# Kernel tuning notes

Measured on AMD Instinct MI355X. Metric: run time of the kernel, lower is better.

Reference implementation:

```python
import jax, jax.numpy as jnp
import numpy as np

N = 8192      # number of input points
K = 16        # nsample for all kNN groupings
STRIDE = 4    # TransitionDown stride -> M = N // 4 output points


def _knn(q, p, k):
    # squared euclidean distances [m, n] -> k nearest indices per query
    d2 = jnp.sum(q * q, 1)[:, None] + jnp.sum(p * p, 1)[None, :] - 2.0 * (q @ p.T)
    return jax.lax.top_k(-d2, k)[1]


def _forward(points, We1, se1, be1, We2, se2, be2,
             Wq1, Wk1, Wv1, sa1, ba1, Wq2, Wk2, Wv2, sa2, ba2,
             Wtd, sd, bd, Wu1, su1, bu1, Wu2, su2, bu2,
             Wc1, bc1, sc, bc, Wc2, bc2):
    p = points[0]                      # [N, 3]
    n = p.shape[0]
    idx = _knn(p, p, K)                # [N, K] shared xyz-kNN (same coords every layer)

    def edge_conv(x, W, s, b):
        # DGCNN EdgeConv: concat(x_i, x_j - x_i) -> Linear -> BN(affine) -> ReLU -> max_k
        xi = x[:, None, :]
        xj = x[idx]                    # [N, K, C]
        e = jnp.concatenate([jnp.broadcast_to(xi, xj.shape), xj - xi], -1)
        h = jax.nn.relu((e @ W) * s + b)
        return h.max(axis=1)

    def graph_attn(x, Wq, Wk, Wv, s, b):
        q, kk, v = x @ Wq, x @ Wk, x @ Wv
        kj, vj = kk[idx], v[idx]       # [N, K, D]
        logits = jnp.einsum('nd,nkd->nk', q, kj) / jnp.sqrt(jnp.float32(q.shape[-1]))
        a = jax.nn.softmax(logits, axis=-1)
        y = jnp.einsum('nk,nkd->nd', a, vj)
        return jax.nn.relu(y * s + b)

    x = edge_conv(p, We1, se1, be1)            # 3 -> 64
    x = edge_conv(x, We2, se2, be2)            # 64 -> 128
    x = graph_attn(x, Wq1, Wk1, Wv1, sa1, ba1) # 128 -> 256
    x = graph_attn(x, Wq2, Wk2, Wv2, sa2, ba2) # 256 -> 512

    # TransitionDown: subsample n/stride points, group kNN with relative xyz, MLP, max-pool
    sel = jnp.arange(0, n, STRIDE)
    pm = p[sel]                                 # [M, 3]
    idx_d = _knn(pm, p, K)                      # [M, K]
    g = jnp.concatenate([p[idx_d] - pm[:, None, :], x[idx_d]], -1)  # [M, K, 3+512]
    xd = jax.nn.relu((g @ Wtd) * sd + bd).max(axis=1)               # [M, 512]

    # TransitionUp(x, o): local linear + broadcast per-cloud pooled branch (single cloud, o=[n])
    gmean = xd.mean(axis=0, keepdims=True)
    xu = jax.nn.relu((xd @ Wu1) * su1 + bu1 + (gmean @ Wu2) * su2 + bu2)  # [M, 256]

    # classifier (eval mode: dropout = identity, BN folded to affine)
    h = jax.nn.relu(((xu @ Wc1) + bc1) * sc + bc)
    return h @ Wc2 + bc2               # [M, num_classes]


def setup_inputs() -> dict:
    key = jax.random.key(0)
    ks = iter(jax.random.split(key, 64))
    def w(shape):
        return jax.random.normal(next(ks), shape, jnp.float32) / jnp.sqrt(jnp.float32(shape[0]))
    def s(d):
        return 1.0 + 0.01 * jax.random.normal(next(ks), (d,), jnp.float32)
    def b(d):
        return 0.01 * jax.random.normal(next(ks), (d,), jnp.float32)
    return {
        'points': jax.random.normal(next(ks), (1, N, 3), jnp.float32),
        'We1': w((6, 64)), 'se1': s(64), 'be1': b(64),
        'We2': w((128, 128)), 'se2': s(128), 'be2': b(128),
        'Wq1': w((128, 256)), 'Wk1': w((128, 256)), 'Wv1': w((128, 256)), 'sa1': s(256), 'ba1': b(256),
        'Wq2': w((256, 512)), 'Wk2': w((256, 512)), 'Wv2': w((256, 512)), 'sa2': s(512), 'ba2': b(512),
        'Wtd': w((515, 512)), 'sd': s(512), 'bd': b(512),
        'Wu1': w((512, 256)), 'su1': s(256), 'bu1': b(256),
        'Wu2': w((512, 256)), 'su2': s(256), 'bu2': b(256),
        'Wc1': w((256, 128)), 'bc1': b(128), 'sc': s(128), 'bc': b(128),
        'Wc2': w((128, 6)), 'bc2': b(6),
    }


def reference(points, We1, se1, be1, We2, se2, be2,
              Wq1, Wk1, Wv1, sa1, ba1, Wq2, Wk2, Wv2, sa2, ba2,
              Wtd, sd, bd, Wu1, su1, bu1, Wu2, su2, bu2,
              Wc1, bc1, sc, bc, Wc2, bc2):
    return _forward(points, We1, se1, be1, We2, se2, be2,
                    Wq1, Wk1, Wv1, sa1, ba1, Wq2, Wk2, Wv2, sa2, ba2,
                    Wtd, sd, bd, Wu1, su1, bu1, Wu2, su2, bu2,
                    Wc1, bc1, sc, bc, Wc2, bc2)
```

## Files before the change

### kernel.cpp

```cpp
#include <hip/hip_runtime.h>


#define NP 8192
#define NDOWN 2048
#define KCAP 64

typedef unsigned long long u64;
typedef __attribute__((ext_vector_type(8))) _Float16 half8;
typedef __attribute__((ext_vector_type(4))) unsigned short us4;
typedef __attribute__((ext_vector_type(8))) unsigned short ushort8;
typedef __attribute__((ext_vector_type(4))) float f32x4;

__device__ __forceinline__ bool lexless(float ad, int ai, float bd, int bi) {
  return ad < bd || (ad == bd && ai < bi);
}

__device__ __forceinline__ unsigned short f2h(float x) {
  _Float16 h = (_Float16)x;
  return __builtin_bit_cast(unsigned short, h);
}
__device__ __forceinline__ float h2f(unsigned short u) {
  return (float)__builtin_bit_cast(_Float16, u);
}

__global__ __launch_bounds__(256) void prep_points_k(const float* __restrict__ pts,
                                                     float4* __restrict__ soa) {
  int i = blockIdx.x * 256 + threadIdx.x;
  float x = pts[3 * i], y = pts[3 * i + 1], z = pts[3 * i + 2];
  soa[i] = make_float4(x, y, z, x * x + y * y + z * z);
}

__global__ __launch_bounds__(256) void wsplit_k(
    const float* __restrict__ We2, const float* __restrict__ Wq1,
    const float* __restrict__ Wk1, const float* __restrict__ Wv1,
    const float* __restrict__ Wq2, const float* __restrict__ Wk2,
    const float* __restrict__ Wv2, const float* __restrict__ Wtd,
    const float* __restrict__ Wu1, const float* __restrict__ Wc1,
    unsigned short* __restrict__ whi) {
  int t = blockIdx.x * 256 + threadIdx.x;
  float v;
  if (t < 16384) {
    int n = t >> 6, k = t & 63;
    if (n < 128) v = We2[k * 128 + n] - We2[(k + 64) * 128 + n];
    else         v = We2[(k + 64) * 128 + (n - 128)];
  } else if (t < 114688) {
    int e = t - 16384;
    int n = e >> 7, k = e & 127;
    if (n < 256)      v = Wq1[k * 256 + n];
    else if (n < 512) v = Wk1[k * 256 + (n - 256)];
    else              v = Wv1[k * 256 + (n - 512)];
  } else if (t < 507904) {
    int e = t - 114688;
    int n = e >> 8, k = e & 255;
    if (n < 512)       v = Wq2[k * 512 + n];
    else if (n < 1024) v = Wk2[k * 512 + (n - 512)];
    else               v = Wv2[k * 512 + (n - 1024)];
  } else if (t < 770048) {
    int e = t - 507904;
    int n = e >> 9, k = e & 511;
    v = Wtd[(3 + k) * 512 + n];
  } else if (t < 901120) {
    int e = t - 770048;
    int n = e >> 9, k = e & 511;
    v = Wu1[k * 256 + n];
  } else {
    int e = t - 901120;
    int n = e >> 8, k = e & 255;
    v = Wc1[k * 128 + n];
  }
  whi[t] = f2h(v);
}

__device__ __forceinline__ void bitonic_val64(float& d, int lane) {
#pragma unroll
  for (int k = 2; k <= 64; k <<= 1) {
#pragma unroll
    for (int j = k >> 1; j >= 1; j >>= 1) {
      float od = __shfl_xor(d, j);
      bool takeMin = (((lane & k) == 0) == ((lane & j) == 0));
      d = takeMin ? fminf(d, od) : fmaxf(d, od);
    }
  }
}

__device__ __forceinline__ void bitonic_lex64(float& d, int& i, int lane) {
#pragma unroll
  for (int k = 2; k <= 64; k <<= 1) {
#pragma unroll
    for (int j = k >> 1; j >= 1; j >>= 1) {
      float od = __shfl_xor(d, j);
      int oi = __shfl_xor(i, j);
      bool takeMin = (((lane & k) == 0) == ((lane & j) == 0));
      bool less = lexless(od, oi, d, i);
      if (takeMin == less) { d = od; i = oi; }
    }
  }
}

__device__ __forceinline__ void insert1(float cd, int ci, int lane,
                                        float& td, int& ti) {
  int p = __popcll(__ballot(lexless(td, ti, cd, ci)));
  if (p < 16) {
    float ud = __shfl_up(td, 1);
    int ui = __shfl_up(ti, 1);
    float ntd = td; int nti = ti;
    if (lane > p && lane < 16) { ntd = ud; nti = ui; }
    if (lane == p) { ntd = cd; nti = ci; }
    td = ntd; ti = nti;
  }
}

__global__ __launch_bounds__(512) void knn_k(const float4* __restrict__ soa,
                                             int* __restrict__ idxout) {
  __shared__ float4 sp[2048];
  __shared__ float cb_d[8][KCAP];
  __shared__ int cb_i[8][KCAP];
  __shared__ int ccnt[8];
  const int lane = threadIdx.x & 63;
  const int wid = threadIdx.x >> 6;
  const int q = blockIdx.x * 8 + wid;
  const float4 qp = soa[q];
  const float qx2 = -2.f * qp.x, qy2 = -2.f * qp.y, qz2 = -2.f * qp.z;
  const float INF = __int_as_float(0x7f800000);
  if (lane == 0) ccnt[wid] = 0;

  float md = INF;
  for (int ch = 0; ch < 4; ++ch) {
    __syncthreads();
    for (int j = 0; j < 4; ++j) {
      int e = j * 512 + threadIdx.x;
      sp[e] = soa[ch * 2048 + e];
    }
    __syncthreads();
#pragma unroll 4
    for (int c = 0; c < 32; ++c) {
      const float4 P = sp[c * 64 + lane];
      float m = fmaf(qx2, P.x, qp.w);
      m = fmaf(qy2, P.y, m);
      m = fmaf(qz2, P.z, m);
      md = fminf(md, m + P.w);
    }
  }
  float sv = md;
  bitonic_val64(sv, lane);
  const float tau = __shfl(sv, 15);
  const float tauM = tau + fabsf(tau) * 1e-5f + 1e-12f;

  for (int ch = 0; ch < 4; ++ch) {
    __syncthreads();
    for (int j = 0; j < 4; ++j) {
      int e = j * 512 + threadIdx.x;
      sp[e] = soa[ch * 2048 + e];
    }
    __syncthreads();
#pragma unroll 4
    for (int c = 0; c < 32; ++c) {
      const float4 P = sp[c * 64 + lane];
      float m = fmaf(qx2, P.x, qp.w);
      m = fmaf(qy2, P.y, m);
      m = fmaf(qz2, P.z, m);
      const float d = m + P.w;
      if (d <= tauM) {
        int slot = atomicAdd(&ccnt[wid], 1);
        if (slot < KCAP) {
          cb_d[wid][slot] = d;
          cb_i[wid][slot] = ch * 2048 + c * 64 + lane;
        }
      }
    }
  }
  int n = ccnt[wid];
  if (n <= KCAP) {
    float dd = (lane < n) ? cb_d[wid][lane] : INF;
    int ii = (lane < n) ? cb_i[wid][lane] : 0x7fffffff;
    bitonic_lex64(dd, ii, lane);
    if (lane < 16) idxout[q * 16 + lane] = ii & 8191;
  } else {
    float td = INF; int ti = 0x7fffffff;
    float Td = INF; int Ti = 0x7fffffff;
    for (int base = 0; base < 8192; base += 64) {
      const float4 P = soa[base + lane];
      float m = fmaf(qx2, P.x, qp.w);
      m = fmaf(qy2, P.y, m);
      m = fmaf(qz2, P.z, m);
      const float d = m + P.w;
      const int gidx = base + lane;
      u64 mk = __ballot(d <= tauM && lexless(d, gidx, Td, Ti));
      while (mk) {
        int s = (int)__builtin_ctzll(mk);
        mk &= mk - 1;
        float cd = __shfl(d, s);
        int ci = __shfl(gidx, s);
        insert1(cd, ci, lane, td, ti);
      }
      Td = __shfl(td, 15); Ti = __shfl(ti, 15);
    }
    if (lane < 16) idxout[q * 16 + lane] = ti & 8191;
  }
}

__global__ __launch_bounds__(256) void proj1_k(const float4* __restrict__ soa,
                                               const float* __restrict__ We1,
                                               float* __restrict__ bz1) {
  int t = blockIdx.x * 256 + threadIdx.x;
  int i = t >> 7, c = t & 127;
  float4 P = soa[i];
  float v;
  if (c < 64) {
    v = P.x * (We1[c] - We1[192 + c]) + P.y * (We1[64 + c] - We1[256 + c]) +
        P.z * (We1[128 + c] - We1[320 + c]);
  } else {
    int cc = c & 63;
    v = P.x * We1[192 + cc] + P.y * We1[256 + cc] + P.z * We1[320 + cc];
  }
  bz1[t] = v;
}

template <int C>
__global__ __launch_bounds__(256) void ec_gm_k(const float* __restrict__ bz,
                                               const int* __restrict__ idx,
                                               const float* __restrict__ s,
                                               const float* __restrict__ b,
                                               unsigned short* __restrict__ xo) {
  constexpr int C4 = C / 4;
  int t = blockIdx.x * 256 + threadIdx.x;
  int i = t / C4, q = t % C4;
  float4 base = *(const float4*)&bz[(size_t)i * (2 * C) + q * 4];
  float4 scl = *(const float4*)&s[q * 4];
  float4 bia = *(const float4*)&b[q * 4];
  float ax = 0.f, ay = 0.f, az = 0.f, aw = 0.f;
  const int* ip = idx + i * 16;
#pragma unroll
  for (int n = 0; n < 16; ++n) {
    int j = ip[n];
    float4 z = *(const float4*)&bz[(size_t)j * (2 * C) + C + q * 4];
    ax = fmaxf(ax, (base.x + z.x) * scl.x + bia.x);
    ay = fmaxf(ay, (base.y + z.y) * scl.y + bia.y);
    az = fmaxf(az, (base.z + z.z) * scl.z + bia.z);
    aw = fmaxf(aw, (base.w + z.w) * scl.w + bia.w);
  }
  us4 o;
  o[0] = f2h(ax); o[1] = f2h(ay); o[2] = f2h(az); o[3] = f2h(aw);
  *(us4*)&xo[(size_t)i * C + q * 4] = o;
}

template <int C>
__global__ __launch_bounds__(256) void attn_fused_k(const float* __restrict__ qf,
                                                    const unsigned short* __restrict__ kvb,
                                                    const int* __restrict__ idx,
                                                    const float* __restrict__ s,
                                                    const float* __restrict__ b,
                                                    unsigned short* __restrict__ xo,
                                                    float scale) {
  int i = blockIdx.x * 4 + (threadIdx.x >> 6);
  int lane = threadIdx.x & 63;
  constexpr int G = C / 256;
  int jreg = (lane < 16) ? idx[i * 16 + lane] : 0;
  float4 qv[G];
#pragma unroll
  for (int g = 0; g < G; ++g)
    qv[g] = *(const float4*)&qf[(size_t)i * C + 4 * lane + 256 * g];
  float lg[16];
#pragma unroll
  for (int n = 0; n < 16; ++n) {
    int j = __shfl(jreg, n);
    const unsigned short* kr = kvb + (size_t)j * (2 * C);
    float ssum = 0.f;
#pragma unroll
    for (int g = 0; g < G; ++g) {
      us4 kk = *(const us4*)&kr[4 * lane + 256 * g];
      ssum += qv[g].x * h2f(kk[0]) + qv[g].y * h2f(kk[1]) +
              qv[g].z * h2f(kk[2]) + qv[g].w * h2f(kk[3]);
    }
    lg[n] = ssum;
  }
#pragma unroll
  for (int n = 0; n < 16; ++n) {
    float vv = lg[n];
    for (int o = 32; o >= 1; o >>= 1) vv += __shfl_xor(vv, o);
    lg[n] = vv * scale;
  }
  float m = lg[0];
#pragma unroll
  for (int n = 1; n < 16; ++n) m = fmaxf(m, lg[n]);
  float ssum = 0.f;
#pragma unroll
  for (int n = 0; n < 16; ++n) { lg[n] = __expf(lg[n] - m); ssum += lg[n]; }
  float inv = 1.f / ssum;
#pragma unroll
  for (int n = 0; n < 16; ++n) lg[n] *= inv;

  float acc[4 * G];
#pragma unroll
  for (int e = 0; e < 4 * G; ++e) acc[e] = 0.f;
#pragma unroll
  for (int n = 0; n < 16; ++n) {
    int j = __shfl(jreg, n);
    const unsigned short* vr = kvb + (size_t)j * (2 * C) + C;
    float w = lg[n];
#pragma unroll
    for (int g = 0; g < G; ++g) {
      us4 v4 = *(const us4*)&vr[4 * lane + 256 * g];
      acc[4 * g + 0] += w * h2f(v4[0]);
      acc[4 * g + 1] += w * h2f(v4[1]);
      acc[4 * g + 2] += w * h2f(v4[2]);
      acc[4 * g + 3] += w * h2f(v4[3]);
    }
  }
#pragma unroll
  for (int g = 0; g < G; ++g) {
    int c0 = 4 * lane + 256 * g;
    float4 scl = *(const float4*)&s[c0];
    float4 bia = *(const float4*)&b[c0];
    us4 o;
    o[0] = f2h(fmaxf(acc[4 * g + 0] * scl.x + bia.x, 0.f));
    o[1] = f2h(fmaxf(acc[4 * g + 1] * scl.y + bia.y, 0.f));
    o[2] = f2h(fmaxf(acc[4 * g + 2] * scl.z + bia.z, 0.f));
    o[3] = f2h(fmaxf(acc[4 * g + 3] * scl.w + bia.w, 0.f));
    *(us4*)&xo[(size_t)i * C + c0] = o;
  }
}

__global__ __launch_bounds__(256) void down_gm_k(const float* __restrict__ vbuf,
                                                 const float4* __restrict__ soa,
                                                 const float* __restrict__ Wtd,
                                                 const int* __restrict__ idx,
                                                 const float* __restrict__ sd,
                                                 const float* __restrict__ bd,
                                                 unsigned short* __restrict__ xd) {
  int t = blockIdx.x * 256 + threadIdx.x;
  int i = t >> 7, q = t & 127;
  int qi = 4 * i;
  float4 qp = soa[qi];
  float4 w0 = *(const float4*)&Wtd[q * 4];
  float4 w1 = *(const float4*)&Wtd[512 + q * 4];
  float4 w2 = *(const float4*)&Wtd[1024 + q * 4];
  float px = qp.x * w0.x + qp.y * w1.x + qp.z * w2.x;
  float py = qp.x * w0.y + qp.y * w1.y + qp.z * w2.y;
  float pz = qp.x * w0.z + qp.y * w1.z + qp.z * w2.z;
  float pw2 = qp.x * w0.w + qp.y * w1.w + qp.z * w2.w;
  float4 scl = *(const float4*)&sd[q * 4];
  float4 bia = *(const float4*)&bd[q * 4];
  float ax = 0.f, ay = 0.f, az = 0.f, aw = 0.f;
  const int* ip = idx + qi * 16;
#pragma unroll
  for (int n = 0; n < 16; ++n) {
    int j = ip[n];
    float4 v = *(const float4*)&vbuf[(size_t)j * 512 + q * 4];
    ax = fmaxf(ax, (v.x - px) * scl.x + bia.x);
    ay = fmaxf(ay, (v.y - py) * scl.y + bia.y);
    az = fmaxf(az, (v.z - pz) * scl.z + bia.z);
    aw = fmaxf(aw, (v.w - pw2) * scl.w + bia.w);
  }
  us4 o;
  o[0] = f2h(ax); o[1] = f2h(ay); o[2] = f2h(az); o[3] = f2h(aw);
  *(us4*)&xd[(size_t)i * 512 + q * 4] = o;
}

__global__ __launch_bounds__(512) void colsum_k(const unsigned short* __restrict__ xd,
                                                float* __restrict__ part) {
  int b = blockIdx.x;
  int c = threadIdx.x;
  float s = 0.f;
  for (int r = b * 128; r < (b + 1) * 128; ++r) s += h2f(xd[(size_t)r * 512 + c]);
  part[b * 512 + c] = s;
}

__global__ __launch_bounds__(256) void gterm_k(const float* __restrict__ part,
                                               const float* __restrict__ Wu2,
                                               const float* __restrict__ su2,
                                               const float* __restrict__ bu2,
                                               float* __restrict__ gterm) {
  __shared__ float gm[512];
  int tid = threadIdx.x;
  for (int c = tid; c < 512; c += 256) {
    float s = 0.f;
#pragma unroll
    for (int b = 0; b < 16; ++b) s += part[b * 512 + c];
    gm[c] = s * (1.f / 2048.f);
  }
  __syncthreads();
  int o = blockIdx.x * 16 + (tid >> 4);
  int kseg = tid & 15;
  float s = 0.f;
#pragma unroll 8
  for (int k = kseg * 32; k < kseg * 32 + 32; ++k) s += gm[k] * Wu2[k * 256 + o];
  s += __shfl_xor(s, 1);
  s += __shfl_xor(s, 2);
  s += __shfl_xor(s, 4);
  s += __shfl_xor(s, 8);
  if (kseg == 0) gterm[o] = s * su2[o] + bu2[o];
}

#define LDSROW 80
template <int MODE>
__global__ __launch_bounds__(256) void gemm_mfma(
    const unsigned short* __restrict__ A,
    const unsigned short* __restrict__ B,
    float* __restrict__ Cf, unsigned short* __restrict__ Ch,
    int M, int N, int K,
    const float4* __restrict__ soaD, const float* __restrict__ wtd,
    const float* __restrict__ s1, const float* __restrict__ b1,
    const float* __restrict__ s2, int Cq, unsigned short* __restrict__ kvb) {
  __shared__ __align__(16) char smem[2 * 128 * LDSROW];
  char* A_s = smem;
  char* B_s = smem + 128 * LDSROW;

  const int tid = threadIdx.x;
  const int lane = tid & 63;
  const int wid = tid >> 6;
  const int wm = wid >> 1, wn = wid & 1;
  const int bm = blockIdx.y * 128, bn = blockIdx.x * 128;
  const int r16 = lane & 15, kb = lane >> 4;

  f32x4 acc[4][4];
#pragma unroll
  for (int a = 0; a < 4; ++a)
#pragma unroll
    for (int b = 0; b < 4; ++b) acc[a][b] = (f32x4)(0.f);

  for (int k0 = 0; k0 < K; k0 += 32) {
    __syncthreads();
#pragma unroll
    for (int qq = 0; qq < 2; ++qq) {
      int idx8 = qq * 256 + tid;
      int row = idx8 >> 2, sq = idx8 & 3;
      size_t goA = (size_t)(bm + row) * K + k0 + sq * 8;
      size_t goB = (size_t)(bn + row) * K + k0 + sq * 8;
      ushort8 a_v = *(const ushort8*)&A[goA];
      ushort8 b_v = *(const ushort8*)&B[goB];
      *(ushort8*)(A_s + row * LDSROW + sq * 16) = a_v;
      *(ushort8*)(B_s + row * LDSROW + sq * 16) = b_v;
    }
    __syncthreads();

    half8 ah[4];
#pragma unroll
    for (int mi = 0; mi < 4; ++mi) {
      int off = (wm * 64 + mi * 16 + r16) * LDSROW + kb * 16;
      ah[mi] = *(const half8*)(A_s + off);
    }
#pragma unroll
    for (int ni = 0; ni < 4; ++ni) {
      int off = (wn * 64 + ni * 16 + r16) * LDSROW + kb * 16;
      half8 bh = *(const half8*)(B_s + off);
#pragma unroll
      for (int mi = 0; mi < 4; ++mi) {
        acc[mi][ni] = __builtin_amdgcn_mfma_f32_16x16x32_f16(ah[mi], bh, acc[mi][ni], 0, 0, 0);
      }
    }
  }

#pragma unroll
  for (int mi = 0; mi < 4; ++mi) {
#pragma unroll
    for (int ni = 0; ni < 4; ++ni) {
      int r0 = bm + wm * 64 + mi * 16 + (lane >> 4) * 4;
      int cc = bn + wn * 64 + ni * 16 + (lane & 15);
      float w0 = 0.f, w1 = 0.f, w2 = 0.f;
      if (MODE == 1) { w0 = wtd[cc]; w1 = wtd[512 + cc]; w2 = wtd[1024 + cc]; }
#pragma unroll
      for (int j = 0; j < 4; ++j) {
        float vv = acc[mi][ni][j];
        int row = r0 + j;
        if (MODE == 1) {
          float4 P = soaD[row];
          vv += P.x * w0 + P.y * w1 + P.z * w2;
        }
        if (MODE == 2) vv = fmaxf(vv * s1[cc] + b1[cc] + s2[cc], 0.f);
        if (MODE == 3) vv = fmaxf((vv + b1[cc]) * s1[cc] + s2[cc], 0.f);
        if (MODE == 2) {
          Ch[(size_t)row * N + cc] = f2h(vv);
        } else if (MODE == 4) {
          if (cc < Cq) Cf[(size_t)row * Cq + cc] = vv;
          else kvb[(size_t)row * (2 * Cq) + (cc - Cq)] = f2h(vv);
        } else {
          Cf[(size_t)row * N + cc] = vv;
        }
      }
    }
  }
}

__global__ __launch_bounds__(256) void out_k(const float* __restrict__ h,
                                             const float* __restrict__ Wc2,
                                             const float* __restrict__ bc2,
                                             float* __restrict__ out) {
  int t = blockIdx.x * 256 + threadIdx.x;
  int pair = t >> 2, kq = t & 3;
  int i = pair / 6, o = pair % 6;
  float s = 0.f;
#pragma unroll 8
  for (int m = kq * 32; m < kq * 32 + 32; ++m) s += h[i * 128 + m] * Wc2[m * 6 + o];
  s += __shfl_xor(s, 1);
  s += __shfl_xor(s, 2);
  if (kq == 0) out[pair] = s + bc2[o];
}

extern "C" void kernel_launch(void* const* d_in, const int* in_sizes, int n_in,
                              void* d_out, int out_size, void* d_ws, size_t ws_size,
                              hipStream_t stream) {
  const float* pts = (const float*)d_in[0];
  const float* We1 = (const float*)d_in[1];
  const float* se1 = (const float*)d_in[2];
  const float* be1 = (const float*)d_in[3];
  const float* We2 = (const float*)d_in[4];
  const float* se2 = (const float*)d_in[5];
  const float* be2 = (const float*)d_in[6];
  const float* Wq1 = (const float*)d_in[7];
  const float* Wk1 = (const float*)d_in[8];
  const float* Wv1 = (const float*)d_in[9];
  const float* sa1 = (const float*)d_in[10];
  const float* ba1 = (const float*)d_in[11];
  const float* Wq2 = (const float*)d_in[12];
  const float* Wk2 = (const float*)d_in[13];
  const float* Wv2 = (const float*)d_in[14];
  const float* sa2 = (const float*)d_in[15];
  const float* ba2 = (const float*)d_in[16];
  const float* Wtd = (const float*)d_in[17];
  const float* sd  = (const float*)d_in[18];
  const float* bd  = (const float*)d_in[19];
  const float* Wu1 = (const float*)d_in[20];
  const float* su1 = (const float*)d_in[21];
  const float* bu1 = (const float*)d_in[22];
  const float* Wu2 = (const float*)d_in[23];
  const float* su2 = (const float*)d_in[24];
  const float* bu2 = (const float*)d_in[25];
  const float* Wc1 = (const float*)d_in[26];
  const float* bc1 = (const float*)d_in[27];
  const float* sc  = (const float*)d_in[28];
  const float* bc  = (const float*)d_in[29];
  const float* Wc2 = (const float*)d_in[30];
  const float* bc2 = (const float*)d_in[31];

  float* ws = (float*)d_ws;
  if (ws_size < (size_t)16703744 * 4) return;
  float* soa   = ws;
  int*   idx   = (int*)(ws + 32768);
  float* gpart = ws + 294912;
  float* gterm = ws + 303104;
  unsigned short* wthi = (unsigned short*)(ws + 303360);
  unsigned short* x1   = (unsigned short*)(ws + 1237248);
  unsigned short* x2   = (unsigned short*)(ws + 1499392);
  unsigned short* x3   = (unsigned short*)(ws + 2023680);
  unsigned short* x4   = (unsigned short*)(ws + 3072256);
  unsigned short* xd   = (unsigned short*)(ws + 5169408);
  unsigned short* xu   = (unsigned short*)(ws + 5693696);
  float* bufP  = ws + 5955840;
  float* qf    = ws + 8052992;
  unsigned short* kvb = (unsigned short*)(ws + 12247296);
  float* hbuf  = ws + 16441600;

  prep_points_k<<<32, 256, 0, stream>>>(pts, (float4*)soa);
  wsplit_k<<<3648, 256, 0, stream>>>(We2, Wq1, Wk1, Wv1, Wq2, Wk2, Wv2, Wtd, Wu1, Wc1, wthi);
  knn_k<<<1024, 512, 0, stream>>>((const float4*)soa, idx);

  proj1_k<<<4096, 256, 0, stream>>>((const float4*)soa, We1, bufP);
  ec_gm_k<64><<<512, 256, 0, stream>>>(bufP, idx, se1, be1, x1);

  gemm_mfma<0><<<dim3(2, 64), 256, 0, stream>>>(x1, wthi,
      bufP, nullptr, NP, 256, 64, nullptr, nullptr, nullptr, nullptr, nullptr, 0, nullptr);
  ec_gm_k<128><<<1024, 256, 0, stream>>>(bufP, idx, se2, be2, x2);

  gemm_mfma<4><<<dim3(6, 64), 256, 0, stream>>>(x2, wthi + 16384,
      qf, nullptr, NP, 768, 128, nullptr, nullptr, nullptr, nullptr, nullptr, 256, kvb);
  attn_fused_k<256><<<2048, 256, 0, stream>>>(qf, kvb, idx, sa1, ba1, x3, 0.0625f);

  gemm_mfma<4><<<dim3(12, 64), 256, 0, stream>>>(x3, wthi + 114688,
      qf, nullptr, NP, 1536, 256, nullptr, nullptr, nullptr, nullptr, nullptr, 512, kvb);
  attn_fused_k<512><<<2048, 256, 0, stream>>>(qf, kvb, idx, sa2, ba2, x4, 0.04419417382415922f);

  gemm_mfma<1><<<dim3(4, 64), 256, 0, stream>>>(x4, wthi + 507904,
      qf, nullptr, NP, 512, 512, (const float4*)soa, Wtd, nullptr, nullptr, nullptr, 0, nullptr);
  down_gm_k<<<1024, 256, 0, stream>>>(qf, (const float4*)soa, Wtd, idx, sd, bd, xd);

  colsum_k<<<16, 512, 0, stream>>>(xd, gpart);
  gterm_k<<<16, 256, 0, stream>>>(gpart, Wu2, su2, bu2, gterm);

  gemm_mfma<2><<<dim3(2, 16), 256, 0, stream>>>(xd, wthi + 770048,
      nullptr, xu, NDOWN, 256, 512, nullptr, nullptr, su1, bu1, gterm, 0, nullptr);
  gemm_mfma<3><<<dim3(1, 16), 256, 0, stream>>>(xu, wthi + 901120,
      hbuf, nullptr, NDOWN, 128, 256, nullptr, nullptr, sc, bc1, bc, 0, nullptr);
  out_k<<<192, 256, 0, stream>>>(hbuf, Wc2, bc2, (float*)d_out);
}
```

Baseline: 266.6 us.

## Process two kNN queries per wavefront and seed top-16 from per-lane minima

The kNN kernel now gives each wavefront two query points, so every point loaded from shared memory is reused for two distance computations, and the grid is halved. The first pass tracks each lane's nearest point with its index. Those 64 lane minima are bitonic-sorted to seed the top-16 list directly, and the second pass only collects the other candidates under the threshold. Those candidates are inserted one at a time with insert1 rather than by a full bitonic sort, and the candidate buffer shrinks to 32 entries. The trade-off is more register pressure, serial insertion loops, and a higher chance of falling back to the slow full-scan path if a threshold admits more than 32 candidates.

```diff
diff --git a/kernel.cpp b/kernel.cpp
--- a/kernel.cpp
+++ b/kernel.cpp
@@ -3,7 +3,7 @@
 
 #define NP 8192
 #define NDOWN 2048
-#define KCAP 64
+#define KCAP 32
 
 typedef unsigned long long u64;
 typedef __attribute__((ext_vector_type(8))) _Float16 half8;
@@ -71,18 +71,6 @@
   whi[t] = f2h(v);
 }
 
-__device__ __forceinline__ void bitonic_val64(float& d, int lane) {
-#pragma unroll
-  for (int k = 2; k <= 64; k <<= 1) {
-#pragma unroll
-    for (int j = k >> 1; j >= 1; j >>= 1) {
-      float od = __shfl_xor(d, j);
-      bool takeMin = (((lane & k) == 0) == ((lane & j) == 0));
-      d = takeMin ? fminf(d, od) : fmaxf(d, od);
-    }
-  }
-}
-
 __device__ __forceinline__ void bitonic_lex64(float& d, int& i, int lane) {
 #pragma unroll
   for (int k = 2; k <= 64; k <<= 1) {
@@ -113,18 +101,21 @@
 __global__ __launch_bounds__(512) void knn_k(const float4* __restrict__ soa,
                                              int* __restrict__ idxout) {
   __shared__ float4 sp[2048];
-  __shared__ float cb_d[8][KCAP];
-  __shared__ int cb_i[8][KCAP];
-  __shared__ int ccnt[8];
+  __shared__ float cb_d[16][KCAP];
+  __shared__ int cb_i[16][KCAP];
+  __shared__ int ccnt[16];
   const int lane = threadIdx.x & 63;
   const int wid = threadIdx.x >> 6;
-  const int q = blockIdx.x * 8 + wid;
-  const float4 qp = soa[q];
-  const float qx2 = -2.f * qp.x, qy2 = -2.f * qp.y, qz2 = -2.f * qp.z;
+  const int q0 = blockIdx.x * 16 + wid * 2;
+  const float4 qa = soa[q0];
+  const float4 qb = soa[q0 + 1];
+  const float ax2 = -2.f * qa.x, ay2 = -2.f * qa.y, az2 = -2.f * qa.z;
+  const float bx2 = -2.f * qb.x, by2 = -2.f * qb.y, bz2 = -2.f * qb.z;
   const float INF = __int_as_float(0x7f800000);
-  if (lane == 0) ccnt[wid] = 0;
-
-  float md = INF;
+  if (lane < 2) ccnt[wid * 2 + lane] = 0;
+
+  float mda = INF, mdb = INF;
+  int mia = 0x7fffffff, mib = 0x7fffffff;
   for (int ch = 0; ch < 4; ++ch) {
     __syncthreads();
     for (int j = 0; j < 4; ++j) {
@@ -135,16 +126,34 @@
 #pragma unroll 4
     for (int c = 0; c < 32; ++c) {
       const float4 P = sp[c * 64 + lane];
-      float m = fmaf(qx2, P.x, qp.w);
-      m = fmaf(qy2, P.y, m);
-      m = fmaf(qz2, P.z, m);
-      md = fminf(md, m + P.w);
-    }
-  }
-  float sv = md;
-  bitonic_val64(sv, lane);
-  const float tau = __shfl(sv, 15);
-  const float tauM = tau + fabsf(tau) * 1e-5f + 1e-12f;
+      const int gidx = ch * 2048 + c * 64 + lane;
+      float da = fmaf(ax2, P.x, qa.w);
+      da = fmaf(ay2, P.y, da);
+      da = fmaf(az2, P.z, da);
+      da += P.w;
+      float db = fmaf(bx2, P.x, qb.w);
+      db = fmaf(by2, P.y, db);
+      db = fmaf(bz2, P.z, db);
+      db += P.w;
+      if (da < mda) { mda = da; mia = gidx; }
+      if (db < mdb) { mdb = db; mib = gidx; }
+    }
+  }
+  const int owna = mia;
+  const int ownb = mib;
+  float sda = mda; int sia = mia;
+  float sdb = mdb; int sib = mib;
+  bitonic_lex64(sda, sia, lane);
+  bitonic_lex64(sdb, sib, lane);
+
+  float tda = (lane < 16) ? sda : INF;
+  int tia = (lane < 16) ? sia : 0x7fffffff;
+  float tdb = (lane < 16) ? sdb : INF;
+  int tib = (lane < 16) ? sib : 0x7fffffff;
+  float Tda = __shfl(sda, 15); int Tia = __shfl(sia, 15);
+  float Tdb = __shfl(sdb, 15); int Tib = __shfl(sib, 15);
+  const float taua = Tda + fabsf(Tda) * 1e-5f + 1e-12f;
+  const float taub = Tdb + fabsf(Tdb) * 1e-5f + 1e-12f;
 
   for (int ch = 0; ch < 4; ++ch) {
     __syncthreads();
@@ -156,46 +165,89 @@
 #pragma unroll 4
     for (int c = 0; c < 32; ++c) {
       const float4 P = sp[c * 64 + lane];
-      float m = fmaf(qx2, P.x, qp.w);
-      m = fmaf(qy2, P.y, m);
-      m = fmaf(qz2, P.z, m);
-      const float d = m + P.w;
-      if (d <= tauM) {
-        int slot = atomicAdd(&ccnt[wid], 1);
-        if (slot < KCAP) {
-          cb_d[wid][slot] = d;
-          cb_i[wid][slot] = ch * 2048 + c * 64 + lane;
-        }
-      }
-    }
-  }
-  int n = ccnt[wid];
-  if (n <= KCAP) {
-    float dd = (lane < n) ? cb_d[wid][lane] : INF;
-    int ii = (lane < n) ? cb_i[wid][lane] : 0x7fffffff;
-    bitonic_lex64(dd, ii, lane);
-    if (lane < 16) idxout[q * 16 + lane] = ii & 8191;
+      const int gidx = ch * 2048 + c * 64 + lane;
+      float da = fmaf(ax2, P.x, qa.w);
+      da = fmaf(ay2, P.y, da);
+      da = fmaf(az2, P.z, da);
+      da += P.w;
+      float db = fmaf(bx2, P.x, qb.w);
+      db = fmaf(by2, P.y, db);
+      db = fmaf(bz2, P.z, db);
+      db += P.w;
+      if (da <= taua && gidx != owna) {
+        int slot = atomicAdd(&ccnt[wid * 2], 1);
+        if (slot < KCAP) { cb_d[wid * 2][slot] = da; cb_i[wid * 2][slot] = gidx; }
+      }
+      if (db <= taub && gidx != ownb) {
+        int slot = atomicAdd(&ccnt[wid * 2 + 1], 1);
+        if (slot < KCAP) { cb_d[wid * 2 + 1][slot] = db; cb_i[wid * 2 + 1][slot] = gidx; }
+      }
+    }
+  }
+
+  int na = ccnt[wid * 2];
+  if (na <= KCAP) {
+    for (int k2 = 0; k2 < na; ++k2) {
+      float cd = cb_d[wid * 2][k2];
+      int ci = cb_i[wid * 2][k2];
+      if (lexless(cd, ci, Tda, Tia)) {
+        insert1(cd, ci, lane, tda, tia);
+        Tda = __shfl(tda, 15); Tia = __shfl(tia, 15);
+      }
+    }
   } else {
-    float td = INF; int ti = 0x7fffffff;
-    float Td = INF; int Ti = 0x7fffffff;
+    tda = INF; tia = 0x7fffffff; Tda = INF; Tia = 0x7fffffff;
     for (int base = 0; base < 8192; base += 64) {
       const float4 P = soa[base + lane];
-      float m = fmaf(qx2, P.x, qp.w);
-      m = fmaf(qy2, P.y, m);
-      m = fmaf(qz2, P.z, m);
-      const float d = m + P.w;
+      float d = fmaf(ax2, P.x, qa.w);
+      d = fmaf(ay2, P.y, d);
+      d = fmaf(az2, P.z, d);
+      d += P.w;
       const int gidx = base + lane;
-      u64 mk = __ballot(d <= tauM && lexless(d, gidx, Td, Ti));
+      u64 mk = __ballot(d <= taua && lexless(d, gidx, Tda, Tia));
       while (mk) {
         int s = (int)__builtin_ctzll(mk);
         mk &= mk - 1;
         float cd = __shfl(d, s);
         int ci = __shfl(gidx, s);
-        insert1(cd, ci, lane, td, ti);
-      }
-      Td = __shfl(td, 15); Ti = __shfl(ti, 15);
-    }
-    if (lane < 16) idxout[q * 16 + lane] = ti & 8191;
+        insert1(cd, ci, lane, tda, tia);
+      }
+      Tda = __shfl(tda, 15); Tia = __shfl(tia, 15);
+    }
+  }
+  int nb = ccnt[wid * 2 + 1];
+  if (nb <= KCAP) {
+    for (int k2 = 0; k2 < nb; ++k2) {
+      float cd = cb_d[wid * 2 + 1][k2];
+      int ci = cb_i[wid * 2 + 1][k2];
+      if (lexless(cd, ci, Tdb, Tib)) {
+        insert1(cd, ci, lane, tdb, tib);
+        Tdb = __shfl(tdb, 15); Tib = __shfl(tib, 15);
+      }
+    }
+  } else {
+    tdb = INF; tib = 0x7fffffff; Tdb = INF; Tib = 0x7fffffff;
+    for (int base = 0; base < 8192; base += 64) {
+      const float4 P = soa[base + lane];
+      float d = fmaf(bx2, P.x, qb.w);
+      d = fmaf(by2, P.y, d);
+      d = fmaf(bz2, P.z, d);
+      d += P.w;
+      const int gidx = base + lane;
+      u64 mk = __ballot(d <= taub && lexless(d, gidx, Tdb, Tib));
+      while (mk) {
+        int s = (int)__builtin_ctzll(mk);
+        mk &= mk - 1;
+        float cd = __shfl(d, s);
+        int ci = __shfl(gidx, s);
+        insert1(cd, ci, lane, tdb, tib);
+      }
+      Tdb = __shfl(tdb, 15); Tib = __shfl(tib, 15);
+    }
+  }
+  if (lane < 16) {
+    idxout[q0 * 16 + lane] = tia & 8191;
+    idxout[(q0 + 1) * 16 + lane] = tib & 8191;
   }
 }
 
@@ -553,7 +605,7 @@
 
   prep_points_k<<<32, 256, 0, stream>>>(pts, (float4*)soa);
   wsplit_k<<<3648, 256, 0, stream>>>(We2, Wq1, Wk1, Wv1, Wq2, Wk2, Wv2, Wtd, Wu1, Wc1, wthi);
-  knn_k<<<1024, 512, 0, stream>>>((const float4*)soa, idx);
+  knn_k<<<512, 512, 0, stream>>>((const float4*)soa, idx);
 
   proj1_k<<<4096, 256, 0, stream>>>((const float4*)soa, We1, bufP);
   ec_gm_k<64><<<512, 256, 0, stream>>>(bufP, idx, se1, be1, x1);
```

Result: faster. 249.7 us (-6.3%).
